# Performance work log

Hardware: AMD Instinct MI355X
Metric: run time of the kernel (lower is better)

The kernel has to match this reference:

```python
import jax, jax.numpy as jnp
import numpy as np


def setup_inputs() -> dict:
    key = jax.random.key(0)
    k1, k2 = jax.random.split(key)
    B, C, H, W = 4, 128, 192, 192
    x = jax.random.normal(k1, (B, C, H, W), dtype=jnp.float32)
    y = jax.random.normal(k2, (B, C, H, W), dtype=jnp.float32)
    return {"x": x, "y": y, "kernel_size": 9, "stride": 1}


def reference(x, y, kernel_size, stride):
    # FlowNet-style correlation volume: for each displacement offset in a
    # kernel_size x kernel_size window (spacing = stride), compute the
    # channel-mean dot product between x and the shifted y.
    # Output: [B, kernel_size**2, H, W]
    B, C, H, W = x.shape
    d = kernel_size // 2          # displacement radius in offset units
    pad = d * stride              # spatial padding so all shifts are valid
    y_pad = jnp.pad(y, ((0, 0), (0, 0), (pad, pad), (pad, pad)))
    inv_c = jnp.float32(1.0 / C)
    outs = []
    # small fixed loop over kernel_size**2 offsets (81 for k=9); each
    # iteration is a fused elementwise-multiply + channel reduction.
    for i in range(kernel_size):
        for j in range(kernel_size):
            ys = jax.lax.dynamic_slice(
                y_pad, (0, 0, i * stride, j * stride), (B, C, H, W))
            outs.append(jnp.sum(x * ys, axis=1) * inv_c)  # [B, H, W]
    return jnp.stack(outs, axis=1)  # [B, k*k, H, W]
```

## Files before the change

kernel.cpp:

```cpp
#include <hip/hip_runtime.h>

typedef short bf16x8 __attribute__((ext_vector_type(8)));
typedef float f32x4  __attribute__((ext_vector_type(4)));
typedef unsigned short us4 __attribute__((ext_vector_type(4)));

#define NT 512

__device__ __forceinline__ unsigned short f2bf(float f) {
    union { float f; unsigned u; } v; v.f = f;
    unsigned r = v.u + 0x7FFFu + ((v.u >> 16) & 1u);
    return (unsigned short)(r >> 16);
}

__global__ __launch_bounds__(NT, 4)
void corr_mfma(const float* __restrict__ x, const float* __restrict__ y,
               float* __restrict__ out)
{
    constexpr int C = 128, H = 192, W = 192;
    constexpr int HT = 8;
    constexpr int KC = 32;
    constexpr int NCHUNK = C / KC;
    const size_t plane = (size_t)H * W;

    __shared__ __align__(16) unsigned short ylds[16 * 32 * KC];
    __shared__ __align__(16) unsigned short xlds[HT * 16 * KC];
    __shared__ float olds[8 * 144];

    const int bid  = blockIdx.x;
    const int task = (bid & 7) * 144 + (bid >> 3);
    const int wt = task % 12;
    const int r1 = task / 12;
    const int ht = r1 % 24;
    const int b  = r1 / 24;
    const int h0 = ht * HT, w0 = wt * 16;

    const int tid  = threadIdx.x;
    const int wid  = tid >> 6;
    const int lane = tid & 63;
    const int lm   = lane & 15;
    const int lg   = lane >> 4;
    const int sel  = (lm >> 1) & 3;

    const float* xb = x + (size_t)b * C * plane;
    const float* yb = y + (size_t)b * C * plane;

    f32x4 acc[9][2];
#pragma unroll
    for (int i = 0; i < 9; ++i) {
        acc[i][0] = (f32x4){0.f, 0.f, 0.f, 0.f};
        acc[i][1] = (f32x4){0.f, 0.f, 0.f, 0.f};
    }

    for (int ck = 0; ck < NCHUNK; ++ck) {
        const int c0 = ck * KC;
#pragma unroll
        for (int k = 0; k < 6; ++k) {
            const int t   = k * NT + tid;
            const int w   = t % 24;
            const int q   = t / 24;
            const int cg  = q & 7;
            const int row = q >> 3;
            const int hg = h0 - 4 + row;
            const int wg = w0 - 4 + w;
            const int hc = min(max(hg, 0), H - 1);
            const int wc = min(max(wg, 0), W - 1);
            const bool ok = (hg >= 0) & (hg < H) & (wg >= 0) & (wg < W);
            const float* p = yb + (size_t)(c0 + cg * 4) * plane + (size_t)hc * W + wc;
            const float v0 = ok ? p[0]         : 0.f;
            const float v1 = ok ? p[plane]     : 0.f;
            const float v2 = ok ? p[2 * plane] : 0.f;
            const float v3 = ok ? p[3 * plane] : 0.f;
            const us4 pk = { f2bf(v0), f2bf(v1), f2bf(v2), f2bf(v3) };
            const int idx = row * 1024 + w * 32
                          + (((cg >> 1) ^ ((w >> 1) & 3)) << 3) + (cg & 1) * 4;
            *reinterpret_cast<us4*>(&ylds[idx]) = pk;
        }
#pragma unroll
        for (int k = 0; k < 2; ++k) {
            const int t   = k * NT + tid;
            const int w   = t & 15;
            const int cg  = (t >> 4) & 7;
            const int row = t >> 7;
            const float* p = xb + (size_t)(c0 + cg * 4) * plane
                           + (size_t)(h0 + row) * W + (w0 + w);
            const us4 pk = { f2bf(p[0]), f2bf(p[plane]), f2bf(p[2 * plane]), f2bf(p[3 * plane]) };
            const int idx = row * 512 + w * 32
                          + (((cg >> 1) ^ ((w >> 1) & 3)) << 3) + (cg & 1) * 4;
            *reinterpret_cast<us4*>(&xlds[idx]) = pk;
        }
        __syncthreads();
        const bf16x8 a = *reinterpret_cast<const bf16x8*>(
            &xlds[wid * 512 + lm * 32 + ((lg ^ sel) << 3)]);
        const int bbase = wid * 1024 + lm * 32 + ((lg ^ sel) << 3);
#pragma unroll
        for (int dy = 0; dy < 9; ++dy) {
            const bf16x8 b0 = *reinterpret_cast<const bf16x8*>(&ylds[bbase + dy * 1024]);
            const bf16x8 b1 = *reinterpret_cast<const bf16x8*>(&ylds[bbase + dy * 1024 + 512]);
            acc[dy][0] = __builtin_amdgcn_mfma_f32_16x16x32_bf16(a, b0, acc[dy][0], 0, 0, 0);
            acc[dy][1] = __builtin_amdgcn_mfma_f32_16x16x32_bf16(a, b1, acc[dy][1], 0, 0, 0);
        }
        __syncthreads();
    }

    const float invc = 1.0f / (float)C;
    float* my = olds + wid * 144;
    const size_t obase = (size_t)b * 81 * plane + (size_t)(h0 + wid) * W + w0;
#pragma unroll
    for (int dy = 0; dy < 9; ++dy) {
#pragma unroll
        for (int nt = 0; nt < 2; ++nt)
#pragma unroll
            for (int j = 0; j < 4; ++j) {
                const int m  = lg * 4 + j;
                const int dx = lm + nt * 16 - m;
                if (dx >= 0 && dx <= 8)
                    my[dx * 16 + m] = acc[dy][nt][j] * invc;
            }
#pragma unroll
        for (int p = 0; p < 3; ++p) {
            const int idx = p * 64 + lane;
            if (idx < 144) {
                const int dx = idx >> 4, m = idx & 15;
                out[obase + (size_t)(dy * 9 + dx) * plane + m] = my[idx];
            }
        }
    }
}

extern "C" void kernel_launch(void* const* d_in, const int* in_sizes, int n_in,
                              void* d_out, int out_size, void* d_ws, size_t ws_size,
                              hipStream_t stream)
{
    const float* x = (const float*)d_in[0];
    const float* y = (const float*)d_in[1];
    float* out = (float*)d_out;
    corr_mfma<<<1152, NT, 0, stream>>>(x, y, out);
}
```

Baseline: 217.4 us.

## Halve row tile, split dy across wave pairs, and prefetch next channel chunk into registers

The tile shrinks from 8 output rows to 4, so the grid doubles. Each pair of waves splits the 9 vertical displacements 4/5, which cuts the accumulator count per wave. The kernel now software-pipelines the loads: global loads for the next 32-channel chunk are issued into registers while the current chunk runs its MFMAs, and the x operand goes straight from registers with no LDS staging. Offsets are precomputed as 32-bit byte offsets, and the output scatter uses a padded LDS stride. The costs are more halo reload of y from the smaller tiles and extra register pressure from the prefetch buffers.

Result: slower. 236.6 us (+8.8%).

```diff
diff --git a/kernel.cpp b/kernel.cpp
--- a/kernel.cpp
+++ b/kernel.cpp
@@ -1,4 +1,5 @@
 #include <hip/hip_runtime.h>
+#include <hip/hip_bf16.h>
 
 typedef short bf16x8 __attribute__((ext_vector_type(8)));
 typedef float f32x4  __attribute__((ext_vector_type(4)));
@@ -7,121 +8,168 @@
 #define NT 512
 
 __device__ __forceinline__ unsigned short f2bf(float f) {
-    union { float f; unsigned u; } v; v.f = f;
-    unsigned r = v.u + 0x7FFFu + ((v.u >> 16) & 1u);
-    return (unsigned short)(r >> 16);
+    __hip_bfloat16 h = __float2bfloat16(f);
+    return reinterpret_cast<const unsigned short&>(h);
 }
 
 __global__ __launch_bounds__(NT, 4)
-void corr_mfma(const float* __restrict__ x, const float* __restrict__ y,
-               float* __restrict__ out)
+void corr_k(const float* __restrict__ x, const float* __restrict__ y,
+            float* __restrict__ out)
 {
-    constexpr int C = 128, H = 192, W = 192;
-    constexpr int HT = 8;
-    constexpr int KC = 32;
-    constexpr int NCHUNK = C / KC;
-    const size_t plane = (size_t)H * W;
+    constexpr int H = 192, W = 192;
+    const int plane = H * W;
+    const int pl4   = plane * 4;
 
-    __shared__ __align__(16) unsigned short ylds[16 * 32 * KC];
-    __shared__ __align__(16) unsigned short xlds[HT * 16 * KC];
-    __shared__ float olds[8 * 144];
+    __shared__ __align__(16) unsigned short ylds[12 * 32 * 32];
+    __shared__ float olds[8 * 192];
 
     const int bid  = blockIdx.x;
-    const int task = (bid & 7) * 144 + (bid >> 3);
-    const int wt = task % 12;
-    const int r1 = task / 12;
-    const int ht = r1 % 24;
-    const int b  = r1 / 24;
-    const int h0 = ht * HT, w0 = wt * 16;
+    const int task = (bid & 7) * 288 + (bid >> 3);
+    const int ht   = task % 48;
+    const int r1   = task / 48;
+    const int wt   = r1 % 12;
+    const int b    = r1 / 12;
+    const int h0 = ht * 4, w0 = wt * 16;
 
     const int tid  = threadIdx.x;
     const int wid  = tid >> 6;
     const int lane = tid & 63;
-    const int lm   = lane & 15;
-    const int lg   = lane >> 4;
+    const int lm = lane & 15, lg = lane >> 4;
     const int sel  = (lm >> 1) & 3;
+    const int r    = wid >> 1;
+    const int half = wid & 1;
+    const int dy0  = half ? 4 : 0;
 
-    const float* xb = x + (size_t)b * C * plane;
-    const float* yb = y + (size_t)b * C * plane;
+    const unsigned boff = (unsigned)b * 128u * (unsigned)pl4;
 
-    f32x4 acc[9][2];
+    unsigned yoff[5]; int lidx[5]; float okf[5];
 #pragma unroll
-    for (int i = 0; i < 9; ++i) {
+    for (int k = 0; k < 5; ++k) {
+        int t = tid + k * NT;
+        if (t >= 2304) t = tid;
+        const int w = t % 24, q = t / 24;
+        const int cg = q & 7, row = q >> 3;
+        const int hg = h0 - 4 + row, wg = w0 - 4 + w;
+        const int hc = min(max(hg, 0), H - 1);
+        const int wc = min(max(wg, 0), W - 1);
+        okf[k] = ((hg >= 0) & (hg < H) & (wg >= 0) & (wg < W)) ? 1.0f : 0.0f;
+        yoff[k] = boff + (unsigned)(cg * 4) * (unsigned)pl4 + (unsigned)(hc * W + wc) * 4u;
+        lidx[k] = row * 1024 + w * 32 + (((cg >> 1) ^ ((w >> 1) & 3)) << 3) + (cg & 1) * 4;
+    }
+    const unsigned xoff = boff + (unsigned)(lg * 8) * (unsigned)pl4
+                        + (unsigned)((h0 + r) * W + (w0 + lm)) * 4u;
+
+    const char* __restrict__ yB = (const char*)y;
+    const char* __restrict__ xB = (const char*)x;
+
+    float ypf[5][4]; float xpf[8];
+    bf16x8 a;
+    f32x4 acc[5][2];
+#pragma unroll
+    for (int i = 0; i < 5; ++i) {
         acc[i][0] = (f32x4){0.f, 0.f, 0.f, 0.f};
         acc[i][1] = (f32x4){0.f, 0.f, 0.f, 0.f};
     }
 
-    for (int ck = 0; ck < NCHUNK; ++ck) {
-        const int c0 = ck * KC;
+    auto ISSUE = [&](int ck) {
+        const unsigned co = (unsigned)ck * 32u * (unsigned)pl4;
 #pragma unroll
-        for (int k = 0; k < 6; ++k) {
-            const int t   = k * NT + tid;
-            const int w   = t % 24;
-            const int q   = t / 24;
-            const int cg  = q & 7;
-            const int row = q >> 3;
-            const int hg = h0 - 4 + row;
-            const int wg = w0 - 4 + w;
-            const int hc = min(max(hg, 0), H - 1);
-            const int wc = min(max(wg, 0), W - 1);
-            const bool ok = (hg >= 0) & (hg < H) & (wg >= 0) & (wg < W);
-            const float* p = yb + (size_t)(c0 + cg * 4) * plane + (size_t)hc * W + wc;
-            const float v0 = ok ? p[0]         : 0.f;
-            const float v1 = ok ? p[plane]     : 0.f;
-            const float v2 = ok ? p[2 * plane] : 0.f;
-            const float v3 = ok ? p[3 * plane] : 0.f;
-            const us4 pk = { f2bf(v0), f2bf(v1), f2bf(v2), f2bf(v3) };
-            const int idx = row * 1024 + w * 32
-                          + (((cg >> 1) ^ ((w >> 1) & 3)) << 3) + (cg & 1) * 4;
-            *reinterpret_cast<us4*>(&ylds[idx]) = pk;
+        for (int k = 0; k < 4; ++k) {
+            const char* p = yB + (yoff[k] + co);
+#pragma unroll
+            for (int j = 0; j < 4; ++j) ypf[k][j] = *(const float*)(p + j * pl4);
+        }
+        if (tid < 256) {
+            const char* p = yB + (yoff[4] + co);
+#pragma unroll
+            for (int j = 0; j < 4; ++j) ypf[4][j] = *(const float*)(p + j * pl4);
+        }
+        const char* px = xB + (xoff + co);
+#pragma unroll
+        for (int j = 0; j < 8; ++j) xpf[j] = *(const float*)(px + j * pl4);
+    };
+
+    auto CVTWRITE = [&]() {
+#pragma unroll
+        for (int k = 0; k < 4; ++k) {
+            us4 pk = { f2bf(ypf[k][0] * okf[k]), f2bf(ypf[k][1] * okf[k]),
+                       f2bf(ypf[k][2] * okf[k]), f2bf(ypf[k][3] * okf[k]) };
+            *reinterpret_cast<us4*>(&ylds[lidx[k]]) = pk;
+        }
+        if (tid < 256) {
+            us4 pk = { f2bf(ypf[4][0] * okf[4]), f2bf(ypf[4][1] * okf[4]),
+                       f2bf(ypf[4][2] * okf[4]), f2bf(ypf[4][3] * okf[4]) };
+            *reinterpret_cast<us4*>(&ylds[lidx[4]]) = pk;
         }
 #pragma unroll
-        for (int k = 0; k < 2; ++k) {
-            const int t   = k * NT + tid;
-            const int w   = t & 15;
-            const int cg  = (t >> 4) & 7;
-            const int row = t >> 7;
-            const float* p = xb + (size_t)(c0 + cg * 4) * plane
-                           + (size_t)(h0 + row) * W + (w0 + w);
-            const us4 pk = { f2bf(p[0]), f2bf(p[plane]), f2bf(p[2 * plane]), f2bf(p[3 * plane]) };
-            const int idx = row * 512 + w * 32
-                          + (((cg >> 1) ^ ((w >> 1) & 3)) << 3) + (cg & 1) * 4;
-            *reinterpret_cast<us4*>(&xlds[idx]) = pk;
+        for (int j = 0; j < 8; ++j) a[j] = (short)f2bf(xpf[j]);
+    };
+
+    auto COMPUTE = [&]() {
+        const int rbase = (r + dy0) * 1024 + lm * 32 + ((lg ^ sel) << 3);
+#pragma unroll
+        for (int i = 0; i < 4; ++i) {
+            const bf16x8 b0 = *reinterpret_cast<const bf16x8*>(&ylds[rbase + i * 1024]);
+            const bf16x8 b1 = *reinterpret_cast<const bf16x8*>(&ylds[rbase + i * 1024 + 512]);
+            acc[i][0] = __builtin_amdgcn_mfma_f32_16x16x32_bf16(a, b0, acc[i][0], 0, 0, 0);
+            acc[i][1] = __builtin_amdgcn_mfma_f32_16x16x32_bf16(a, b1, acc[i][1], 0, 0, 0);
         }
+        if (half) {
+            const bf16x8 b0 = *reinterpret_cast<const bf16x8*>(&ylds[rbase + 4096]);
+            const bf16x8 b1 = *reinterpret_cast<const bf16x8*>(&ylds[rbase + 4096 + 512]);
+            acc[4][0] = __builtin_amdgcn_mfma_f32_16x16x32_bf16(a, b0, acc[4][0], 0, 0, 0);
+            acc[4][1] = __builtin_amdgcn_mfma_f32_16x16x32_bf16(a, b1, acc[4][1], 0, 0, 0);
+        }
+    };
+
+    ISSUE(0);
+    CVTWRITE();
+    __syncthreads();
+    ISSUE(1);
+    COMPUTE();
+#pragma unroll
+    for (int ck = 1; ck < 4; ++ck) {
         __syncthreads();
-        const bf16x8 a = *reinterpret_cast<const bf16x8*>(
-            &xlds[wid * 512 + lm * 32 + ((lg ^ sel) << 3)]);
-        const int bbase = wid * 1024 + lm * 32 + ((lg ^ sel) << 3);
-#pragma unroll
-        for (int dy = 0; dy < 9; ++dy) {
-            const bf16x8 b0 = *reinterpret_cast<const bf16x8*>(&ylds[bbase + dy * 1024]);
-            const bf16x8 b1 = *reinterpret_cast<const bf16x8*>(&ylds[bbase + dy * 1024 + 512]);
-            acc[dy][0] = __builtin_amdgcn_mfma_f32_16x16x32_bf16(a, b0, acc[dy][0], 0, 0, 0);
-            acc[dy][1] = __builtin_amdgcn_mfma_f32_16x16x32_bf16(a, b1, acc[dy][1], 0, 0, 0);
-        }
+        CVTWRITE();
         __syncthreads();
+        if (ck < 3) ISSUE(ck + 1);
+        COMPUTE();
     }
 
-    const float invc = 1.0f / (float)C;
-    float* my = olds + wid * 144;
-    const size_t obase = (size_t)b * 81 * plane + (size_t)(h0 + wid) * W + w0;
+    const float invc = 1.0f / 128.0f;
+    float* my = olds + wid * 192;
+    int woff[8];
 #pragma unroll
-    for (int dy = 0; dy < 9; ++dy) {
+    for (int q = 0; q < 8; ++q) {
+        const int nt = q >> 2, j = q & 3;
+        const int m = lg * 4 + j;
+        const int dxx = lm + nt * 16 - m;
+        woff[q] = (dxx >= 0 && dxx <= 8) ? dxx * 17 + m : 160 + (lane & 31);
+    }
+    int ridx[3]; unsigned soff[3];
 #pragma unroll
-        for (int nt = 0; nt < 2; ++nt)
+    for (int p = 0; p < 3; ++p) {
+        const int idx = p * 64 + lane;
+        const int dxr = idx >> 4, mr = idx & 15;
+        ridx[p] = dxr * 17 + mr;
+        soff[p] = (unsigned)(dxr * plane + mr) * 4u;
+    }
+    char* ob = (char*)out + ((size_t)b * 81 * plane + (size_t)(h0 + r) * W + w0) * 4;
+
 #pragma unroll
-            for (int j = 0; j < 4; ++j) {
-                const int m  = lg * 4 + j;
-                const int dx = lm + nt * 16 - m;
-                if (dx >= 0 && dx <= 8)
-                    my[dx * 16 + m] = acc[dy][nt][j] * invc;
-            }
+    for (int i = 0; i < 5; ++i) {
+        if (i < 4 || half) {
+            const int dy = dy0 + i;
 #pragma unroll
-        for (int p = 0; p < 3; ++p) {
-            const int idx = p * 64 + lane;
-            if (idx < 144) {
-                const int dx = idx >> 4, m = idx & 15;
-                out[obase + (size_t)(dy * 9 + dx) * plane + m] = my[idx];
+            for (int q = 0; q < 8; ++q)
+                my[woff[q]] = acc[i][q >> 2][q & 3] * invc;
+            const unsigned dyoff = (unsigned)(dy * 9 * plane) * 4u;
+#pragma unroll
+            for (int p = 0; p < 3; ++p) {
+                if (p < 2 || lane < 16) {
+                    const float v = my[ridx[p]];
+                    *(float*)(ob + (size_t)(dyoff + soff[p])) = v;
+                }
             }
         }
     }
@@ -134,5 +182,5 @@
     const float* x = (const float*)d_in[0];
     const float* y = (const float*)d_in[1];
     float* out = (float*)d_out;
-    corr_mfma<<<1152, NT, 0, stream>>>(x, y, out);
+    corr_k<<<2304, NT, 0, stream>>>(x, y, out);
 }
```
